# Performance work log

Measured on AMD Instinct MI355X. Metric: run time of the kernel, lower is better.

Reference implementation:

```python
import jax, jax.numpy as jnp
import numpy as np

B, F, L = 256, 32, 4096  # batch, num_filters, length == input_dim


def setup_inputs() -> dict:
    key = jax.random.key(0)
    k1, k2, k3 = jax.random.split(key, 3)
    x = jax.random.normal(k1, (B, L), dtype=jnp.float32)
    window_params = jax.random.normal(k2, (F, L), dtype=jnp.float32) * 0.02
    # original init: linspace(0.1, 0.5, F).unsqueeze(0); use same deterministic init
    freq_params = jnp.linspace(0.1, 0.5, F, dtype=jnp.float32)[None, :]
    return {"x": x, "window_params": window_params, "freq_params": freq_params}


def reference(x, window_params, freq_params):
    # x: [B, L]; window_params: [F, L]; freq_params: [1, F]
    length = x.shape[-1]
    windows = jax.nn.softmax(window_params, axis=-1)            # [F, L]
    freqs = jax.nn.sigmoid(freq_params)[0] * 0.5                # [F]
    n = jnp.arange(length, dtype=jnp.float32)                   # [L]
    # complex modulation atoms for ALL filters at once (single batched FFT)
    phase = -2.0 * jnp.pi * freqs[:, None] * n[None, :]         # [F, L]
    modulation = jnp.exp(1j * phase.astype(jnp.complex64))      # [F, L] complex64
    atoms = windows.astype(jnp.complex64) * modulation          # [F, L]
    Xf = jnp.fft.fft(x, axis=-1)                                # [B, L]
    Af = jnp.fft.fft(atoms, axis=-1)                            # [F, L]
    # circular correlation of x with each atom, all filters batched
    prod = Xf[:, None, :] * jnp.conj(Af)[None, :, :]            # [B, F, L]
    return jnp.real(jnp.fft.ifft(prod, axis=-1)).astype(x.dtype)  # [B, F, L]
```

## Files before the change

kernel.cpp:

```cpp
#include <hip/hip_runtime.h>
#include <math.h>

#define B 256
#define F 32
#define L 4096
#define NT 256
#define TWO_PI 6.28318530717958647692f

__device__ __forceinline__ int pidx(int i) { return i + (i >> 4); }

__device__ __forceinline__ int rev3(int i) {
    return ((i & 15) << 8) | (i & 0xF0) | (i >> 8);
}

__device__ __forceinline__ float2 cmul(float2 a, float2 b) {
    return make_float2(a.x * b.x - a.y * b.y, a.x * b.y + a.y * b.x);
}
__device__ __forceinline__ float2 cmulc(float2 a, float cr, float ci) {
    return make_float2(a.x * cr - a.y * ci, a.x * ci + a.y * cr);
}

template<int SGN>
__device__ __forceinline__ void dft4(float2& a, float2& b, float2& c, float2& d) {
    const float s = (float)SGN;
    float2 t0 = make_float2(a.x + c.x, a.y + c.y);
    float2 t1 = make_float2(a.x - c.x, a.y - c.y);
    float2 t2 = make_float2(b.x + d.x, b.y + d.y);
    float2 t3 = make_float2(b.x - d.x, b.y - d.y);
    float2 it3 = make_float2(-s * t3.y, s * t3.x);
    a = make_float2(t0.x + t2.x, t0.y + t2.y);
    c = make_float2(t0.x - t2.x, t0.y - t2.y);
    b = make_float2(t1.x + it3.x, t1.y + it3.y);
    d = make_float2(t1.x - it3.x, t1.y - it3.y);
}

template<int SGN>
__device__ __forceinline__ void dft16(float2 v[16]) {
    const float s = (float)SGN;
    const float C1 = 0.92387953251128675613f;
    const float S1 = 0.38268343236508977173f;
    const float C2 = 0.70710678118654752440f;
    #pragma unroll
    for (int c = 0; c < 4; ++c) dft4<SGN>(v[c], v[c + 4], v[c + 8], v[c + 12]);
    v[5]  = cmulc(v[5],  C1,  s * S1);
    v[6]  = cmulc(v[6],  C2,  s * C2);
    v[7]  = cmulc(v[7],  S1,  s * C1);
    v[9]  = cmulc(v[9],  C2,  s * C2);
    v[10] = make_float2(-s * v[10].y, s * v[10].x);
    v[11] = cmulc(v[11], -C2, s * C2);
    v[13] = cmulc(v[13], S1,  s * C1);
    v[14] = cmulc(v[14], -C2, s * C2);
    v[15] = cmulc(v[15], -C1, -s * S1);
    float2 o[16];
    #pragma unroll
    for (int m = 0; m < 4; ++m) {
        float2 a = v[4*m], b = v[4*m+1], c = v[4*m+2], d = v[4*m+3];
        dft4<SGN>(a, b, c, d);
        o[m] = a; o[m+4] = b; o[m+8] = c; o[m+12] = d;
    }
    #pragma unroll
    for (int i = 0; i < 16; ++i) v[i] = o[i];
}

__device__ __forceinline__ void twiddle_pow(float2 v[16], float2 w1) {
    float2 w = w1;
    #pragma unroll
    for (int q = 1; q < 16; ++q) {
        v[q] = cmul(v[q], w);
        w = cmul(w, w1);
    }
}

template<int SGN>
__device__ __forceinline__ void build_tables(float2* twp, float2* T1, int t) {
    float sv, cv;
    float a1 = (float)SGN * (TWO_PI / (float)L) * (float)t;
    sincosf(a1, &sv, &cv);
    twp[pidx(t)] = make_float2(cv, sv);
    float a2 = (float)SGN * (TWO_PI / 256.0f) * (float)((t >> 4) * (t & 15));
    sincosf(a2, &sv, &cv);
    T1[17 * (t >> 4) + (t & 15)] = make_float2(cv, sv);
}

__device__ __forceinline__ void fft_dif_fwd(float2 v[16], float2* lds,
                                            const float2* twp, const float2* T1, int t) {
    dft16<-1>(v);
    twiddle_pow(v, twp[pidx(t)]);
    #pragma unroll
    for (int p = 0; p < 16; ++p) lds[pidx(t + 256 * p)] = v[p];
    __syncthreads();
    const int base = (t >> 4) * 256 + (t & 15);
    #pragma unroll
    for (int q = 0; q < 16; ++q) v[q] = lds[pidx(base + 16 * q)];
    dft16<-1>(v);
    {
        const float2* Tr = T1 + 17 * (t & 15);
        #pragma unroll
        for (int p = 1; p < 16; ++p) v[p] = cmul(v[p], Tr[p]);
    }
    #pragma unroll
    for (int p = 0; p < 16; ++p) lds[pidx(base + 16 * p)] = v[p];
    __syncthreads();
    #pragma unroll
    for (int q = 0; q < 16; ++q) v[q] = lds[pidx(16 * t + q)];
    dft16<-1>(v);
}

__global__ void __launch_bounds__(NT) prep_kernel(const float* __restrict__ x,
                                                  const float* __restrict__ wp,
                                                  const float* __restrict__ fp,
                                                  float2* __restrict__ Xs,
                                                  float2* __restrict__ Anat) {
    __shared__ float2 lds[L + (L >> 4)];
    __shared__ float2 twp[272];
    __shared__ float2 T1[272];
    __shared__ float red[4];
    const int t = threadIdx.x;
    build_tables<-1>(twp, T1, t);
    float2 v[16];

    if (blockIdx.x < F) {
        const int f = blockIdx.x;
        const float* row = wp + (size_t)f * L;
        float rv[16];
        #pragma unroll
        for (int c = 0; c < 16; ++c) rv[c] = row[t + 256 * c];
        float m = -INFINITY;
        #pragma unroll
        for (int c = 0; c < 16; ++c) m = fmaxf(m, rv[c]);
        #pragma unroll
        for (int off = 32; off; off >>= 1) m = fmaxf(m, __shfl_down(m, off));
        if ((t & 63) == 0) red[t >> 6] = m;
        __syncthreads();
        m = fmaxf(fmaxf(red[0], red[1]), fmaxf(red[2], red[3]));
        __syncthreads();
        float s = 0.0f;
        #pragma unroll
        for (int c = 0; c < 16; ++c) { rv[c] = expf(rv[c] - m); s += rv[c]; }
        #pragma unroll
        for (int off = 32; off; off >>= 1) s += __shfl_down(s, off);
        if ((t & 63) == 0) red[t >> 6] = s;
        __syncthreads();
        s = red[0] + red[1] + red[2] + red[3];
        const float inv = 1.0f / s;
        const float fr = 0.5f / (1.0f + expf(-fp[f]));
        const float w0 = -TWO_PI * fr;
        #pragma unroll
        for (int c = 0; c < 16; ++c) {
            const int n = t + 256 * c;
            const float e = rv[c] * inv;
            float sv, cv;
            sincosf(w0 * (float)n, &sv, &cv);
            v[c] = make_float2(e * cv, e * sv);
        }
        __syncthreads();
        fft_dif_fwd(v, lds, twp, T1, t);
        float2* an = Anat + (size_t)f * L;
        #pragma unroll
        for (int r = 0; r < 16; ++r) an[rev3(16 * t + r)] = v[r];
    } else {
        const int bb = blockIdx.x - F;
        const float* row = x + (size_t)bb * L;
        #pragma unroll
        for (int q = 0; q < 16; ++q) v[q] = make_float2(row[t + 256 * q], 0.0f);
        __syncthreads();
        fft_dif_fwd(v, lds, twp, T1, t);
        float4* o4 = (float4*)(Xs + (size_t)bb * L + 16 * t);
        #pragma unroll
        for (int h = 0; h < 8; ++h)
            o4[h] = make_float4(v[2*h].x, v[2*h].y, v[2*h+1].x, v[2*h+1].y);
    }
}

__global__ void __launch_bounds__(NT) pair_kernel(const float2* __restrict__ Anat,
                                                  float2* __restrict__ Cs) {
    const int j = blockIdx.x;
    const int t = threadIdx.x;
    const float2* a0 = Anat + (size_t)(2 * j) * L;
    const float2* a1 = a0 + L;
    const float sc = 0.5f / (float)L;
    float2* co = Cs + (size_t)j * L;
    #pragma unroll
    for (int c = 0; c < 16; ++c) {
        const int i = t + 256 * c;
        const int k = rev3(i);
        const int km = (L - k) & (L - 1);
        const float2 a0k = a0[k], a0m = a0[km];
        const float2 a1k = a1[k], a1m = a1[km];
        const float g0r = a0k.x + a0m.x, g0i = a0m.y - a0k.y;
        const float g1r = a1k.x + a1m.x, g1i = a1m.y - a1k.y;
        co[i] = make_float2((g0r - g1i) * sc, (g0i + g1r) * sc);
    }
}

__global__ void __launch_bounds__(NT, 4) corr_kernel(const float2* __restrict__ Xs,
                                                     const float2* __restrict__ Cs,
                                                     float* __restrict__ out) {
    __shared__ float2 lds[L + (L >> 4)];
    __shared__ float2 twp[272];
    __shared__ float2 T1[272];
    const int blk = blockIdx.x;
    const int jf = (blk >> 3) & 15;
    const int b = ((blk >> 7) << 3) | (blk & 7);
    const int t = threadIdx.x;

    const float4* x4 = (const float4*)(Xs + (size_t)b * L + 16 * t);
    const float4* c4 = (const float4*)(Cs + (size_t)jf * L + 16 * t);
    float4 xa[8], ca[8];
    #pragma unroll
    for (int h = 0; h < 8; ++h) { xa[h] = x4[h]; ca[h] = c4[h]; }

    build_tables<1>(twp, T1, t);

    float2 v[16];
    #pragma unroll
    for (int h = 0; h < 8; ++h) {
        v[2*h]   = cmul(make_float2(xa[h].x, xa[h].y), make_float2(ca[h].x, ca[h].y));
        v[2*h+1] = cmul(make_float2(xa[h].z, xa[h].w), make_float2(ca[h].z, ca[h].w));
    }
    dft16<1>(v);
    #pragma unroll
    for (int r = 0; r < 16; ++r) lds[pidx(16 * t + r)] = v[r];
    __syncthreads();
    {
        const int base = (t >> 4) * 256 + (t & 15);
        const float2* Tr = T1 + 17 * (t & 15);
        #pragma unroll
        for (int q = 0; q < 16; ++q) v[q] = lds[pidx(base + 16 * q)];
        #pragma unroll
        for (int q = 1; q < 16; ++q) v[q] = cmul(v[q], Tr[q]);
        dft16<1>(v);
        #pragma unroll
        for (int r = 0; r < 16; ++r) lds[pidx(base + 16 * r)] = v[r];
    }
    __syncthreads();
    #pragma unroll
    for (int q = 0; q < 16; ++q) v[q] = lds[pidx(t + 256 * q)];
    twiddle_pow(v, twp[pidx(t)]);
    dft16<1>(v);
    float* o0 = out + ((size_t)b * F + 2 * jf) * L;
    float* o1 = o0 + L;
    #pragma unroll
    for (int r = 0; r < 16; ++r) {
        __builtin_nontemporal_store(v[r].x, o0 + t + 256 * r);
        __builtin_nontemporal_store(v[r].y, o1 + t + 256 * r);
    }
}

extern "C" void kernel_launch(void* const* d_in, const int* in_sizes, int n_in,
                              void* d_out, int out_size, void* d_ws, size_t ws_size,
                              hipStream_t stream) {
    (void)in_sizes; (void)n_in; (void)out_size; (void)ws_size;
    const float* x  = (const float*)d_in[0];
    const float* wp = (const float*)d_in[1];
    const float* fp = (const float*)d_in[2];
    float* out = (float*)d_out;

    float2* Xs   = (float2*)d_ws;
    float2* Cs   = Xs + (size_t)B * L;
    float2* Anat = Cs + (size_t)(F / 2) * L;

    prep_kernel<<<dim3(F + B), dim3(NT), 0, stream>>>(x, wp, fp, Xs, Anat);
    pair_kernel<<<dim3(F / 2), dim3(NT), 0, stream>>>(Anat, Cs);
    corr_kernel<<<dim3(B * F / 2), dim3(NT), 0, stream>>>(Xs, Cs, out);
}
```

Before: 181.7 us.

## Pack two real signal FFTs per complex FFT and compute twiddles in registers

Result: no change. 182.6 us (+0.5%).

```diff
diff --git a/kernel.cpp b/kernel.cpp
--- a/kernel.cpp
+++ b/kernel.cpp
@@ -72,20 +72,19 @@
 }
 
 template<int SGN>
-__device__ __forceinline__ void build_tables(float2* twp, float2* T1, int t) {
+__device__ __forceinline__ void gen_tw(int t, float2& w1, float2& u1) {
     float sv, cv;
-    float a1 = (float)SGN * (TWO_PI / (float)L) * (float)t;
-    sincosf(a1, &sv, &cv);
-    twp[pidx(t)] = make_float2(cv, sv);
-    float a2 = (float)SGN * (TWO_PI / 256.0f) * (float)((t >> 4) * (t & 15));
-    sincosf(a2, &sv, &cv);
-    T1[17 * (t >> 4) + (t & 15)] = make_float2(cv, sv);
-}
-
-__device__ __forceinline__ void fft_dif_fwd(float2 v[16], float2* lds,
-                                            const float2* twp, const float2* T1, int t) {
+    sincosf((float)SGN * (TWO_PI / (float)L) * (float)t, &sv, &cv);
+    w1 = make_float2(cv, sv);
+    sincosf((float)SGN * (TWO_PI / 256.0f) * (float)(t & 15), &sv, &cv);
+    u1 = make_float2(cv, sv);
+}
+
+__device__ __forceinline__ void fft_dif_fwd(float2 v[16], float2* lds, int t) {
+    float2 w1, u1;
+    gen_tw<-1>(t, w1, u1);
     dft16<-1>(v);
-    twiddle_pow(v, twp[pidx(t)]);
+    twiddle_pow(v, w1);
     #pragma unroll
     for (int p = 0; p < 16; ++p) lds[pidx(t + 256 * p)] = v[p];
     __syncthreads();
@@ -93,14 +92,9 @@
     #pragma unroll
     for (int q = 0; q < 16; ++q) v[q] = lds[pidx(base + 16 * q)];
     dft16<-1>(v);
-    {
-        const float2* Tr = T1 + 17 * (t & 15);
-        #pragma unroll
-        for (int p = 1; p < 16; ++p) v[p] = cmul(v[p], Tr[p]);
-    }
+    twiddle_pow(v, u1);
     #pragma unroll
     for (int p = 0; p < 16; ++p) lds[pidx(base + 16 * p)] = v[p];
-    __syncthreads();
     #pragma unroll
     for (int q = 0; q < 16; ++q) v[q] = lds[pidx(16 * t + q)];
     dft16<-1>(v);
@@ -109,14 +103,11 @@
 __global__ void __launch_bounds__(NT) prep_kernel(const float* __restrict__ x,
                                                   const float* __restrict__ wp,
                                                   const float* __restrict__ fp,
-                                                  float2* __restrict__ Xs,
+                                                  float2* __restrict__ Znat,
                                                   float2* __restrict__ Anat) {
     __shared__ float2 lds[L + (L >> 4)];
-    __shared__ float2 twp[272];
-    __shared__ float2 T1[272];
     __shared__ float red[4];
     const int t = threadIdx.x;
-    build_tables<-1>(twp, T1, t);
     float2 v[16];
 
     if (blockIdx.x < F) {
@@ -153,43 +144,60 @@
             sincosf(w0 * (float)n, &sv, &cv);
             v[c] = make_float2(e * cv, e * sv);
         }
-        __syncthreads();
-        fft_dif_fwd(v, lds, twp, T1, t);
+        fft_dif_fwd(v, lds, t);
         float2* an = Anat + (size_t)f * L;
         #pragma unroll
         for (int r = 0; r < 16; ++r) an[rev3(16 * t + r)] = v[r];
     } else {
-        const int bb = blockIdx.x - F;
-        const float* row = x + (size_t)bb * L;
-        #pragma unroll
-        for (int q = 0; q < 16; ++q) v[q] = make_float2(row[t + 256 * q], 0.0f);
-        __syncthreads();
-        fft_dif_fwd(v, lds, twp, T1, t);
-        float4* o4 = (float4*)(Xs + (size_t)bb * L + 16 * t);
-        #pragma unroll
-        for (int h = 0; h < 8; ++h)
-            o4[h] = make_float4(v[2*h].x, v[2*h].y, v[2*h+1].x, v[2*h+1].y);
+        const int m = blockIdx.x - F;
+        const float* r0 = x + (size_t)(2 * m) * L;
+        const float* r1 = r0 + L;
+        #pragma unroll
+        for (int q = 0; q < 16; ++q)
+            v[q] = make_float2(r0[t + 256 * q], r1[t + 256 * q]);
+        fft_dif_fwd(v, lds, t);
+        float2* zn = Znat + (size_t)m * L;
+        #pragma unroll
+        for (int r = 0; r < 16; ++r) zn[rev3(16 * t + r)] = v[r];
     }
 }
 
 __global__ void __launch_bounds__(NT) pair_kernel(const float2* __restrict__ Anat,
-                                                  float2* __restrict__ Cs) {
-    const int j = blockIdx.x;
+                                                  const float2* __restrict__ Znat,
+                                                  float2* __restrict__ Cs,
+                                                  float2* __restrict__ Xs) {
     const int t = threadIdx.x;
-    const float2* a0 = Anat + (size_t)(2 * j) * L;
-    const float2* a1 = a0 + L;
-    const float sc = 0.5f / (float)L;
-    float2* co = Cs + (size_t)j * L;
-    #pragma unroll
-    for (int c = 0; c < 16; ++c) {
-        const int i = t + 256 * c;
-        const int k = rev3(i);
-        const int km = (L - k) & (L - 1);
-        const float2 a0k = a0[k], a0m = a0[km];
-        const float2 a1k = a1[k], a1m = a1[km];
-        const float g0r = a0k.x + a0m.x, g0i = a0m.y - a0k.y;
-        const float g1r = a1k.x + a1m.x, g1i = a1m.y - a1k.y;
-        co[i] = make_float2((g0r - g1i) * sc, (g0i + g1r) * sc);
+    if (blockIdx.x < (F / 2)) {
+        const int j = blockIdx.x;
+        const float2* a0 = Anat + (size_t)(2 * j) * L;
+        const float2* a1 = a0 + L;
+        const float sc = 0.5f / (float)L;
+        float2* co = Cs + (size_t)j * L;
+        #pragma unroll
+        for (int c = 0; c < 16; ++c) {
+            const int i = t + 256 * c;
+            const int k = rev3(i);
+            const int km = (L - k) & (L - 1);
+            const float2 a0k = a0[k], a0m = a0[km];
+            const float2 a1k = a1[k], a1m = a1[km];
+            const float g0r = a0k.x + a0m.x, g0i = a0m.y - a0k.y;
+            const float g1r = a1k.x + a1m.x, g1i = a1m.y - a1k.y;
+            co[i] = make_float2((g0r - g1i) * sc, (g0i + g1r) * sc);
+        }
+    } else {
+        const int m = blockIdx.x - (F / 2);
+        const float2* z = Znat + (size_t)m * L;
+        float2* o0 = Xs + (size_t)(2 * m) * L;
+        float2* o1 = o0 + L;
+        #pragma unroll
+        for (int c = 0; c < 16; ++c) {
+            const int i = t + 256 * c;
+            const int k = rev3(i);
+            const int km = (L - k) & (L - 1);
+            const float2 zk = z[k], zm = z[km];
+            o0[i] = make_float2(0.5f * (zk.x + zm.x), 0.5f * (zk.y - zm.y));
+            o1[i] = make_float2(0.5f * (zk.y + zm.y), 0.5f * (zm.x - zk.x));
+        }
     }
 }
 
@@ -197,8 +205,6 @@
                                                      const float2* __restrict__ Cs,
                                                      float* __restrict__ out) {
     __shared__ float2 lds[L + (L >> 4)];
-    __shared__ float2 twp[272];
-    __shared__ float2 T1[272];
     const int blk = blockIdx.x;
     const int jf = (blk >> 3) & 15;
     const int b = ((blk >> 7) << 3) | (blk & 7);
@@ -210,7 +216,8 @@
     #pragma unroll
     for (int h = 0; h < 8; ++h) { xa[h] = x4[h]; ca[h] = c4[h]; }
 
-    build_tables<1>(twp, T1, t);
+    float2 w1, u1;
+    gen_tw<1>(t, w1, u1);
 
     float2 v[16];
     #pragma unroll
@@ -221,22 +228,17 @@
     dft16<1>(v);
     #pragma unroll
     for (int r = 0; r < 16; ++r) lds[pidx(16 * t + r)] = v[r];
+    const int base = (t >> 4) * 256 + (t & 15);
+    #pragma unroll
+    for (int q = 0; q < 16; ++q) v[q] = lds[pidx(base + 16 * q)];
+    twiddle_pow(v, u1);
+    dft16<1>(v);
+    #pragma unroll
+    for (int r = 0; r < 16; ++r) lds[pidx(base + 16 * r)] = v[r];
     __syncthreads();
-    {
-        const int base = (t >> 4) * 256 + (t & 15);
-        const float2* Tr = T1 + 17 * (t & 15);
-        #pragma unroll
-        for (int q = 0; q < 16; ++q) v[q] = lds[pidx(base + 16 * q)];
-        #pragma unroll
-        for (int q = 1; q < 16; ++q) v[q] = cmul(v[q], Tr[q]);
-        dft16<1>(v);
-        #pragma unroll
-        for (int r = 0; r < 16; ++r) lds[pidx(base + 16 * r)] = v[r];
-    }
-    __syncthreads();
     #pragma unroll
     for (int q = 0; q < 16; ++q) v[q] = lds[pidx(t + 256 * q)];
-    twiddle_pow(v, twp[pidx(t)]);
+    twiddle_pow(v, w1);
     dft16<1>(v);
     float* o0 = out + ((size_t)b * F + 2 * jf) * L;
     float* o1 = o0 + L;
@@ -259,8 +261,9 @@
     float2* Xs   = (float2*)d_ws;
     float2* Cs   = Xs + (size_t)B * L;
     float2* Anat = Cs + (size_t)(F / 2) * L;
-
-    prep_kernel<<<dim3(F + B), dim3(NT), 0, stream>>>(x, wp, fp, Xs, Anat);
-    pair_kernel<<<dim3(F / 2), dim3(NT), 0, stream>>>(Anat, Cs);
+    float2* Znat = Anat + (size_t)F * L;
+
+    prep_kernel<<<dim3(F + B / 2), dim3(NT), 0, stream>>>(x, wp, fp, Znat, Anat);
+    pair_kernel<<<dim3(F / 2 + B / 2), dim3(NT), 0, stream>>>(Anat, Znat, Cs, Xs);
     corr_kernel<<<dim3(B * F / 2), dim3(NT), 0, stream>>>(Xs, Cs, out);
 }
```
